# Kernel tuning notes

Measured on AMD Instinct MI355X. Metric: run time of the kernel, lower is better.

## Reference

```python
import jax, jax.numpy as jnp
import numpy as np

N_NODES = 200   # nlim = 50*4
EMB = 5
N_APPTYPES = 3
FEAT_IN = 50 * 52 + N_NODES  # 2800
B = 16384
E = 800


def setup_inputs() -> dict:
    key = jax.random.key(0)
    ks = jax.random.split(key, 16)
    x = jax.random.normal(ks[0], (B, 50, 52), dtype=jnp.float32)
    apps = jax.random.randint(ks[1], (B, N_NODES), 0, N_APPTYPES)
    edge_src = jax.random.randint(ks[2], (E,), 0, N_NODES)
    edge_dst = jax.random.randint(ks[3], (E,), 0, N_NODES)
    def lin(k, fan_in, fan_out):
        bound = 1.0 / np.sqrt(fan_in)
        kw, kb = jax.random.split(k)
        W = jax.random.uniform(kw, (fan_in, fan_out), minval=-bound, maxval=bound, dtype=jnp.float32)
        b = jax.random.uniform(kb, (fan_out,), minval=-bound, maxval=bound, dtype=jnp.float32)
        return W, b
    emb_table = jax.random.normal(ks[4], (N_APPTYPES, EMB), dtype=jnp.float32)
    gc_w, gc_b = lin(ks[5], EMB, 1)
    W1, b1 = lin(ks[6], FEAT_IN, 128)
    W2, b2 = lin(ks[7], 128, 128)
    W3, b3 = lin(ks[8], 128, 64)
    W4, b4 = lin(ks[9], 64, 2)
    return {"x": x, "apps": apps, "edge_src": edge_src, "edge_dst": edge_dst,
            "emb_table": emb_table, "gc_w": gc_w, "gc_b": gc_b,
            "W1": W1, "b1": b1, "W2": W2, "b2": b2,
            "W3": W3, "b3": b3, "W4": W4, "b4": b4}


def _graph_conv(h, edge_src, edge_dst, gc_w, gc_b):
    # DGL GraphConv, norm='both': D_in^{-1/2} A D_out^{-1/2} (X W) + b
    ones = jnp.ones((edge_src.shape[0],), dtype=h.dtype)
    deg_out = jnp.clip(jax.ops.segment_sum(ones, edge_src, num_segments=N_NODES), 1.0)
    deg_in = jnp.clip(jax.ops.segment_sum(ones, edge_dst, num_segments=N_NODES), 1.0)
    norm_src = deg_out ** -0.5  # [N]
    norm_dst = deg_in ** -0.5
    hw = h @ gc_w                       # [B, N, 1] (weight applied first: 5 > 1)
    msg = (hw * norm_src[None, :, None])[:, edge_src, :]      # [B, E, 1]
    agg = jnp.zeros_like(hw).at[:, edge_dst, :].add(msg)      # scatter-add over dst
    return agg * norm_dst[None, :, None] + gc_b


def reference(x, apps, edge_src, edge_dst, emb_table, gc_w, gc_b,
              W1, b1, W2, b2, W3, b3, W4, b4):
    h = emb_table[apps]                 # [B, 200, 5]; apps already length nlim -> zero-pad is no-op
    g = _graph_conv(h, edge_src, edge_dst, gc_w, gc_b)        # [B, 200, 1]
    feat = jnp.concatenate([x.reshape(x.shape[0], -1), g.reshape(g.shape[0], -1)], axis=-1)  # [B, 2800]
    a = jax.nn.softplus(feat @ W1 + b1)
    a = jax.nn.softplus(a @ W2 + b2)
    a = a @ W3 + b3
    a = a - jnp.tanh(a)                 # Tanhshrink
    out = jax.nn.sigmoid(a @ W4 + b4)   # [B, 2]
    return out
```

## Files before the change

kernel.cpp:

```cpp
#include <hip/hip_runtime.h>

#define NNODES 200
#define FEATX  2600
#define FEAT   2800
#define NCH    44
#define N1     128

typedef _Float16 f16;
typedef _Float16 f16x8 __attribute__((ext_vector_type(8)));
typedef float    f32x4 __attribute__((ext_vector_type(4)));

#define W1T_OFF   0u
#define W2T_OFF   720896u
#define W3T_OFF   753664u
#define WG_OFF    770048u
#define B1P_OFF   872448u
#define HW_OFF    872960u
#define WE_OFF    874816u

__device__ __forceinline__ void gl_lds16(const void* g, void* l) {
  __builtin_amdgcn_global_load_lds(
      (const __attribute__((address_space(1))) unsigned int*)g,
      (__attribute__((address_space(3))) unsigned int*)l, 16, 0, 0);
}

__global__ void prep1(const int* __restrict__ esrc, const int* __restrict__ edst,
                      const float* __restrict__ emb, const float* __restrict__ gcw,
                      const float* __restrict__ gcb, const float* __restrict__ W1,
                      const float* __restrict__ b1, char* __restrict__ ws) {
  __shared__ float dg[2][NNODES];
  const int tid = threadIdx.x;
  for (int i = tid; i < 2 * NNODES; i += 256) ((float*)dg)[i] = 0.f;
  __syncthreads();
  for (int e = tid; e < 800; e += 256) {
    atomicAdd(&dg[0][esrc[e]], 1.f);
    atomicAdd(&dg[1][edst[e]], 1.f);
  }
  __syncthreads();
  for (int i = tid; i < 2 * NNODES; i += 256) {
    float* p = (float*)dg + i;
    *p = 1.f / sqrtf(fmaxf(*p, 1.f));
  }
  if (tid < 3) {
    float s = 0.f;
    for (int q = 0; q < 5; ++q) s += emb[tid * 5 + q] * gcw[q];
    ((float*)(ws + HW_OFF))[tid] = s;
  }
  __syncthreads();
  float* we = (float*)(ws + WE_OFF);
  for (int e = tid; e < 800; e += 256)
    we[e] = dg[0][esrc[e]] * dg[1][edst[e]];
  if (tid < 128) {
    float s = 0.f;
    for (int d = 0; d < NNODES; ++d) s += W1[(FEATX + d) * N1 + tid];
    ((float*)(ws + B1P_OFF))[tid] = b1[tid] + gcb[0] * s;
  }
}

__global__ void prepWg(const int* __restrict__ esrc, const int* __restrict__ edst,
                       const float* __restrict__ W1, char* __restrict__ ws) {
  __shared__ int   se[800];
  __shared__ short sd[800];
  __shared__ float swe[800];
  const int n = blockIdx.x;
  const int j = threadIdx.x;
  const float* we = (const float*)(ws + WE_OFF);
  for (int e = j; e < 800; e += 128) {
    se[e] = esrc[e]; sd[e] = (short)edst[e]; swe[e] = we[e];
  }
  __syncthreads();
  float acc = 0.f;
  for (int e = 0; e < 800; ++e) {
    if (se[e] == n) acc += swe[e] * W1[(FEATX + (int)sd[e]) * N1 + j];
  }
  ((float*)(ws + WG_OFF))[n * N1 + j] = acc;
}

__global__ void pack(const float* __restrict__ W1, const float* __restrict__ W2,
                     const float* __restrict__ W3, char* __restrict__ ws) {
  __shared__ __align__(16) char tile[32768];
  const int bid = blockIdx.x, tid = threadIdx.x;
  if (bid < NCH) {
    const float* wg = (const float*)(ws + WG_OFF);
    const int c = tid & 127, kh = tid >> 7;
    for (int kk = kh; kk < 64; kk += 2) {
      const int k = bid * 64 + kk;
      float v;
      if (k < FEATX) v = W1[k * N1 + c];
      else if (k < FEAT) v = wg[(k - FEATX) * N1 + c];
      else v = 0.f;
      *(f16*)(tile + ((c * 128 + kk * 2) ^ ((c & 7) << 4))) = (f16)v;
    }
    __syncthreads();
    char* dst = ws + W1T_OFF + bid * 16384;
    for (int i = 0; i < 4; ++i)
      *(uint4*)(dst + tid * 16 + i * 4096) = *(const uint4*)(tile + tid * 16 + i * 4096);
  } else if (bid == NCH) {
    const int c = tid & 127, kh = tid >> 7;
    for (int k = kh; k < 128; k += 2) {
      const float v = W2[k * 128 + c];
      *(f16*)(tile + ((c * 256 + k * 2) ^ ((c & 7) << 4))) = (f16)v;
    }
    __syncthreads();
    char* dst = ws + W2T_OFF;
    for (int i = 0; i < 8; ++i)
      *(uint4*)(dst + tid * 16 + i * 4096) = *(const uint4*)(tile + tid * 16 + i * 4096);
  } else {
    const int c = tid & 63, kh = tid >> 6;
    for (int k = kh; k < 128; k += 4) {
      const float v = W3[k * 64 + c];
      *(f16*)(tile + ((c * 256 + k * 2) ^ ((c & 7) << 4))) = (f16)v;
    }
    __syncthreads();
    char* dst = ws + W3T_OFF;
    for (int i = 0; i < 4; ++i)
      *(uint4*)(dst + tid * 16 + i * 4096) = *(const uint4*)(tile + tid * 16 + i * 4096);
  }
}

__global__ __launch_bounds__(512, 2)
void fused_main(const float* __restrict__ x, const int* __restrict__ apps,
                const char* __restrict__ ws, const float* __restrict__ b2,
                const float* __restrict__ b3, const float* __restrict__ W4,
                const float* __restrict__ b4, float* __restrict__ out) {
  __shared__ __align__(16) char lds[81920];
  char*  sB    = lds;
  char*  sAct1 = lds + 49152;
  char*  sAct2 = lds + 65536;
  float* sAct3 = (float*)(lds + 49152);

  const int tid  = threadIdx.x;
  const int lane = tid & 63;
  const int w    = tid >> 6;
  const int lrow = lane & 15;
  const int lk   = lane >> 4;
  const int wr   = w >> 1;
  const int wc   = w & 1;
  const int blk  = blockIdx.x;

  const float* hwv = (const float*)(ws + HW_OFF);
  const float hw0 = hwv[0], hw1 = hwv[1], hw2 = hwv[2];

  const int row_g = blk * 64 + wr * 16 + lrow;
  const float* xrow = x + (size_t)row_g * FEATX;
  const int*   irow = apps + (size_t)row_g * NNODES;

  int boff[2][4];
#pragma unroll
  for (int ks = 0; ks < 2; ++ks)
#pragma unroll
    for (int f = 0; f < 4; ++f) {
      const int c = wc * 64 + f * 16 + lrow;
      boff[ks][f] = ((c * 128 + ks * 64 + lk * 16) ^ ((lrow & 7) << 4));
    }

  const f32x4 zed = {0.f, 0.f, 0.f, 0.f};
  f32x4 acc1[4] = {zed, zed, zed, zed};

  auto issueB = [&](int tc, int buf) {
    const char* src = ws + W1T_OFF + (size_t)tc * 16384;
    char* dst = sB + buf * 16384;
#pragma unroll
    for (int r = 0; r < 2; ++r) {
      const int o = r * 8192 + w * 1024;
      gl_lds16(src + o + lane * 16, dst + o);
    }
  };
  auto issueA = [&](int tc, uint4 (&ar)[2][2]) {
#pragma unroll
    for (int ks = 0; ks < 2; ++ks) {
      const int k0 = tc * 64 + ks * 32 + lk * 8;
      const char* p;
      if (k0 + 8 <= FEATX)  p = (const char*)(xrow + k0);
      else if (k0 < FEAT)   p = (const char*)(irow + (k0 - FEATX));
      else                  p = (const char*)xrow;
      ar[ks][0] = *(const uint4*)p;
      ar[ks][1] = *(const uint4*)(p + 16);
    }
  };
  auto cvtA = [&](int t, const uint4 (&ar)[2][2], f16x8 (&af)[2]) {
#pragma unroll
    for (int ks = 0; ks < 2; ++ks) {
      const int k0 = t * 64 + ks * 32 + lk * 8;
      union { uint4 u[2]; unsigned ui[8]; float f[8]; } d;
      d.u[0] = ar[ks][0]; d.u[1] = ar[ks][1];
      union { f16x8 v; f16 h[8]; } r;
      if (k0 + 8 <= FEATX) {
#pragma unroll
        for (int j2 = 0; j2 < 8; ++j2) r.h[j2] = (f16)d.f[j2];
      } else if (k0 < FEAT) {
#pragma unroll
        for (int j2 = 0; j2 < 8; ++j2) {
          const unsigned a = d.ui[j2];
          r.h[j2] = (f16)(a == 0u ? hw0 : (a == 1u ? hw1 : hw2));
        }
      } else {
#pragma unroll
        for (int j2 = 0; j2 < 8; ++j2) r.h[j2] = (f16)0.f;
      }
      af[ks] = r.v;
    }
  };
  auto compute = [&](const f16x8 (&af)[2], int buf) {
    const char* b = sB + buf * 16384;
#pragma unroll
    for (int ks = 0; ks < 2; ++ks)
#pragma unroll
      for (int f = 0; f < 4; ++f) {
        const f16x8 bf = *(const f16x8*)(b + boff[ks][f]);
        acc1[f] = __builtin_amdgcn_mfma_f32_16x16x32_f16(af[ks], bf, acc1[f], 0, 0, 0);
      }
  };

  uint4 arA[2][2], arB[2][2];
  f16x8 af[2];

  issueB(0, 0); issueA(0, arA);
  issueB(1, 1); issueA(1, arB);

  for (int t = 0; t < NCH; t += 2) {
    {
      asm volatile("s_waitcnt vmcnt(6)" ::: "memory");
      __builtin_amdgcn_s_barrier();
      __builtin_amdgcn_sched_barrier(0);
      const int tc = (t + 2 < NCH) ? t + 2 : NCH - 1;
      issueB(tc, (t + 2) % 3);
      cvtA(t, arA, af);
      issueA(tc, arA);
      compute(af, t % 3);
    }
    {
      asm volatile("s_waitcnt vmcnt(6)" ::: "memory");
      __builtin_amdgcn_s_barrier();
      __builtin_amdgcn_sched_barrier(0);
      const int t1 = t + 1;
      const int tc = (t1 + 2 < NCH) ? t1 + 2 : NCH - 1;
      issueB(tc, (t1 + 2) % 3);
      cvtA(t1, arB, af);
      issueA(tc, arB);
      compute(af, t1 % 3);
    }
  }
  __syncthreads();

#pragma unroll
  for (int r = 0; r < 6; ++r) {
    const int o = r * 8192 + w * 1024;
    gl_lds16(ws + W2T_OFF + o + lane * 16, lds + o);
  }

  const float* b1p = (const float*)(ws + B1P_OFF);
#pragma unroll
  for (int f = 0; f < 4; ++f) {
    const int col = wc * 64 + f * 16 + lrow;
    const float bb = b1p[col];
#pragma unroll
    for (int r = 0; r < 4; ++r) {
      const int row = wr * 16 + lk * 4 + r;
      float v = acc1[f][r] + bb;
      v = fmaxf(v, 0.f) + log1pf(expf(-fabsf(v)));
      *(f16*)(sAct1 + ((row * 256 + col * 2) ^ ((row & 7) << 4))) = (f16)v;
    }
  }
  __syncthreads();

  f32x4 acc2[4] = {zed, zed, zed, zed};
#pragma unroll
  for (int ks = 0; ks < 4; ++ks) {
    const int ar = wr * 16 + lrow;
    const f16x8 a2 = *(const f16x8*)(sAct1 + ((ar * 256 + ks * 64 + lk * 16) ^ ((lrow & 7) << 4)));
#pragma unroll
    for (int f = 0; f < 4; ++f) {
      const int c = wc * 64 + f * 16 + lrow;
      const f16x8 bf = *(const f16x8*)(lds + ((c * 256 + ks * 64 + lk * 16) ^ ((lrow & 7) << 4)));
      acc2[f] = __builtin_amdgcn_mfma_f32_16x16x32_f16(a2, bf, acc2[f], 0, 0, 0);
    }
  }
#pragma unroll
  for (int f = 0; f < 4; ++f) {
    const int col = wc * 64 + f * 16 + lrow;
    const float bb = b2[col];
#pragma unroll
    for (int r = 0; r < 4; ++r) {
      const int row = wr * 16 + lk * 4 + r;
      float v = acc2[f][r] + bb;
      v = fmaxf(v, 0.f) + log1pf(expf(-fabsf(v)));
      *(f16*)(sAct2 + ((row * 256 + col * 2) ^ ((row & 7) << 4))) = (f16)v;
    }
  }
  __syncthreads();

  f32x4 acc3[2] = {zed, zed};
  const char* w3p = lds + 32768;
#pragma unroll
  for (int ks = 0; ks < 4; ++ks) {
    const int ar = wr * 16 + lrow;
    const f16x8 a3 = *(const f16x8*)(sAct2 + ((ar * 256 + ks * 64 + lk * 16) ^ ((lrow & 7) << 4)));
#pragma unroll
    for (int f = 0; f < 2; ++f) {
      const int c = wc * 32 + f * 16 + lrow;
      const f16x8 bf = *(const f16x8*)(w3p + ((c * 256 + ks * 64 + lk * 16) ^ ((lrow & 7) << 4)));
      acc3[f] = __builtin_amdgcn_mfma_f32_16x16x32_f16(a3, bf, acc3[f], 0, 0, 0);
    }
  }
#pragma unroll
  for (int f = 0; f < 2; ++f) {
    const int col = wc * 32 + f * 16 + lrow;
    const float bb = b3[col];
#pragma unroll
    for (int r = 0; r < 4; ++r) {
      const int row = wr * 16 + lk * 4 + r;
      const float z = acc3[f][r] + bb;
      sAct3[row * 64 + col] = z - tanhf(z);
    }
  }
  __syncthreads();

  if (tid < 128) {
    const int row = tid >> 1, j = tid & 1;
    float a4 = b4[j];
#pragma unroll 8
    for (int k = 0; k < 64; ++k)
      a4 += sAct3[row * 64 + k] * W4[k * 2 + j];
    out[(size_t)(blk * 64 + row) * 2 + j] = 1.f / (1.f + expf(-a4));
  }
}

extern "C" void kernel_launch(void* const* d_in, const int* in_sizes, int n_in,
                              void* d_out, int out_size, void* d_ws, size_t ws_size,
                              hipStream_t stream) {
  const float* x    = (const float*)d_in[0];
  const int*   apps = (const int*)d_in[1];
  const int*   esrc = (const int*)d_in[2];
  const int*   edst = (const int*)d_in[3];
  const float* emb  = (const float*)d_in[4];
  const float* gcw  = (const float*)d_in[5];
  const float* gcb  = (const float*)d_in[6];
  const float* W1   = (const float*)d_in[7];
  const float* b1   = (const float*)d_in[8];
  const float* W2   = (const float*)d_in[9];
  const float* b2   = (const float*)d_in[10];
  const float* W3   = (const float*)d_in[11];
  const float* b3   = (const float*)d_in[12];
  const float* W4   = (const float*)d_in[13];
  const float* b4   = (const float*)d_in[14];
  char* ws = (char*)d_ws;
  float* out = (float*)d_out;

  hipLaunchKernelGGL(prep1, dim3(1), dim3(256), 0, stream,
                     esrc, edst, emb, gcw, gcb, W1, b1, ws);
  hipLaunchKernelGGL(prepWg, dim3(200), dim3(128), 0, stream, esrc, edst, W1, ws);
  hipLaunchKernelGGL(pack, dim3(46), dim3(256), 0, stream, W1, W2, W3, ws);
  hipLaunchKernelGGL(fused_main, dim3(256), dim3(512), 0, stream,
                     x, apps, ws, b2, b3, W4, b4, out);
}
```

Baseline: 391.4 us.

## Stage W1 in 64KB double-buffered groups and merge graph prep kernels

After: 516.4 us. 1.32x slower.

```diff
diff --git a/kernel.cpp b/kernel.cpp
--- a/kernel.cpp
+++ b/kernel.cpp
@@ -4,6 +4,7 @@
 #define FEATX  2600
 #define FEAT   2800
 #define NCH    44
+#define NGRP   11
 #define N1     128
 
 typedef _Float16 f16;
@@ -16,7 +17,6 @@
 #define WG_OFF    770048u
 #define B1P_OFF   872448u
 #define HW_OFF    872960u
-#define WE_OFF    874816u
 
 __device__ __forceinline__ void gl_lds16(const void* g, void* l) {
   __builtin_amdgcn_global_load_lds(
@@ -24,20 +24,30 @@
       (__attribute__((address_space(3))) unsigned int*)l, 16, 0, 0);
 }
 
-__global__ void prep1(const int* __restrict__ esrc, const int* __restrict__ edst,
-                      const float* __restrict__ emb, const float* __restrict__ gcw,
-                      const float* __restrict__ gcb, const float* __restrict__ W1,
-                      const float* __restrict__ b1, char* __restrict__ ws) {
-  __shared__ float dg[2][NNODES];
+__global__ __launch_bounds__(256)
+void prep(const int* __restrict__ esrc, const int* __restrict__ edst,
+          const float* __restrict__ emb, const float* __restrict__ gcw,
+          const float* __restrict__ gcb, const float* __restrict__ W1,
+          const float* __restrict__ b1, char* __restrict__ ws) {
+  __shared__ float dg[2][256];
+  __shared__ int   se[800];
+  __shared__ int   sd[800];
+  __shared__ float swe[800];
+  __shared__ float wga[NNODES * N1];
+  __shared__ float red[256];
   const int tid = threadIdx.x;
-  for (int i = tid; i < 2 * NNODES; i += 256) ((float*)dg)[i] = 0.f;
+
+  for (int i = tid; i < 512; i += 256) ((float*)dg)[i] = 0.f;
+  for (int i = tid; i < NNODES * N1; i += 256) wga[i] = 0.f;
   __syncthreads();
   for (int e = tid; e < 800; e += 256) {
-    atomicAdd(&dg[0][esrc[e]], 1.f);
-    atomicAdd(&dg[1][edst[e]], 1.f);
-  }
-  __syncthreads();
-  for (int i = tid; i < 2 * NNODES; i += 256) {
+    const int s = esrc[e], d = edst[e];
+    se[e] = s; sd[e] = d;
+    atomicAdd(&dg[0][s], 1.f);
+    atomicAdd(&dg[1][d], 1.f);
+  }
+  __syncthreads();
+  for (int i = tid; i < 512; i += 256) {
     float* p = (float*)dg + i;
     *p = 1.f / sqrtf(fmaxf(*p, 1.f));
   }
@@ -47,33 +57,28 @@
     ((float*)(ws + HW_OFF))[tid] = s;
   }
   __syncthreads();
-  float* we = (float*)(ws + WE_OFF);
   for (int e = tid; e < 800; e += 256)
-    we[e] = dg[0][esrc[e]] * dg[1][edst[e]];
-  if (tid < 128) {
+    swe[e] = dg[0][se[e]] * dg[1][sd[e]];
+  __syncthreads();
+
+  const int j = tid & 127, h = tid >> 7;
+  for (int e = h; e < 800; e += 2) {
+    const float v = swe[e] * W1[(FEATX + sd[e]) * N1 + j];
+    atomicAdd(&wga[se[e] * N1 + j], v);
+  }
+
+  {
     float s = 0.f;
-    for (int d = 0; d < NNODES; ++d) s += W1[(FEATX + d) * N1 + tid];
-    ((float*)(ws + B1P_OFF))[tid] = b1[tid] + gcb[0] * s;
-  }
-}
-
-__global__ void prepWg(const int* __restrict__ esrc, const int* __restrict__ edst,
-                       const float* __restrict__ W1, char* __restrict__ ws) {
-  __shared__ int   se[800];
-  __shared__ short sd[800];
-  __shared__ float swe[800];
-  const int n = blockIdx.x;
-  const int j = threadIdx.x;
-  const float* we = (const float*)(ws + WE_OFF);
-  for (int e = j; e < 800; e += 128) {
-    se[e] = esrc[e]; sd[e] = (short)edst[e]; swe[e] = we[e];
-  }
-  __syncthreads();
-  float acc = 0.f;
-  for (int e = 0; e < 800; ++e) {
-    if (se[e] == n) acc += swe[e] * W1[(FEATX + (int)sd[e]) * N1 + j];
-  }
-  ((float*)(ws + WG_OFF))[n * N1 + j] = acc;
+    for (int d = h; d < NNODES; d += 2)
+      s += W1[(FEATX + d) * N1 + j];
+    red[tid] = s;
+    __syncthreads();
+    if (h == 0)
+      ((float*)(ws + B1P_OFF))[j] = b1[j] + gcb[0] * (red[j] + red[128 + j]);
+  }
+  __syncthreads();
+  float4* dst = (float4*)(ws + WG_OFF);
+  for (int i = tid; i < NNODES * N1 / 4; i += 256) dst[i] = ((const float4*)wga)[i];
 }
 
 __global__ void pack(const float* __restrict__ W1, const float* __restrict__ W2,
@@ -123,8 +128,7 @@
                 const char* __restrict__ ws, const float* __restrict__ b2,
                 const float* __restrict__ b3, const float* __restrict__ W4,
                 const float* __restrict__ b4, float* __restrict__ out) {
-  __shared__ __align__(16) char lds[81920];
-  char*  sB    = lds;
+  __shared__ __align__(16) char lds[131072];
   char*  sAct1 = lds + 49152;
   char*  sAct2 = lds + 65536;
   float* sAct3 = (float*)(lds + 49152);
@@ -157,11 +161,12 @@
   const f32x4 zed = {0.f, 0.f, 0.f, 0.f};
   f32x4 acc1[4] = {zed, zed, zed, zed};
 
-  auto issueB = [&](int tc, int buf) {
-    const char* src = ws + W1T_OFF + (size_t)tc * 16384;
-    char* dst = sB + buf * 16384;
-#pragma unroll
-    for (int r = 0; r < 2; ++r) {
+  auto issueG = [&](int g) {
+    const int gg = (g > NGRP - 1) ? NGRP - 1 : g;
+    const char* src = ws + W1T_OFF + (size_t)(gg * 4) * 16384;
+    char* dst = lds + (g & 1) * 65536;
+#pragma unroll
+    for (int r = 0; r < 8; ++r) {
       const int o = r * 8192 + w * 1024;
       gl_lds16(src + o + lane * 16, dst + o);
     }
@@ -201,8 +206,7 @@
       af[ks] = r.v;
     }
   };
-  auto compute = [&](const f16x8 (&af)[2], int buf) {
-    const char* b = sB + buf * 16384;
+  auto compute = [&](const f16x8 (&af)[2], const char* b) {
 #pragma unroll
     for (int ks = 0; ks < 2; ++ks)
 #pragma unroll
@@ -215,31 +219,32 @@
   uint4 arA[2][2], arB[2][2];
   f16x8 af[2];
 
-  issueB(0, 0); issueA(0, arA);
-  issueB(1, 1); issueA(1, arB);
-
-  for (int t = 0; t < NCH; t += 2) {
-    {
-      asm volatile("s_waitcnt vmcnt(6)" ::: "memory");
-      __builtin_amdgcn_s_barrier();
-      __builtin_amdgcn_sched_barrier(0);
-      const int tc = (t + 2 < NCH) ? t + 2 : NCH - 1;
-      issueB(tc, (t + 2) % 3);
-      cvtA(t, arA, af);
-      issueA(tc, arA);
-      compute(af, t % 3);
-    }
-    {
-      asm volatile("s_waitcnt vmcnt(6)" ::: "memory");
-      __builtin_amdgcn_s_barrier();
-      __builtin_amdgcn_sched_barrier(0);
-      const int t1 = t + 1;
-      const int tc = (t1 + 2 < NCH) ? t1 + 2 : NCH - 1;
-      issueB(tc, (t1 + 2) % 3);
-      cvtA(t1, arB, af);
-      issueA(tc, arB);
-      compute(af, t1 % 3);
-    }
+  issueG(0);
+  __builtin_amdgcn_sched_barrier(0);
+  issueA(0, arA);
+  issueA(1, arB);
+  __builtin_amdgcn_sched_barrier(0);
+
+  for (int g = 0; g < NGRP; ++g) {
+    asm volatile("s_waitcnt vmcnt(8)" ::: "memory");
+    __builtin_amdgcn_s_barrier();
+    __builtin_amdgcn_sched_barrier(0);
+    issueG(g + 1);
+    __builtin_amdgcn_sched_barrier(0);
+    const char* bb = lds + (g & 1) * 65536;
+    const int t0 = 4 * g;
+    cvtA(t0 + 0, arA, af); issueA(t0 + 2, arA);
+    __builtin_amdgcn_sched_barrier(0);
+    compute(af, bb);
+    cvtA(t0 + 1, arB, af); issueA(t0 + 3, arB);
+    __builtin_amdgcn_sched_barrier(0);
+    compute(af, bb + 16384);
+    cvtA(t0 + 2, arA, af); issueA(t0 + 4, arA);
+    __builtin_amdgcn_sched_barrier(0);
+    compute(af, bb + 32768);
+    cvtA(t0 + 3, arB, af); issueA(t0 + 5, arB);
+    __builtin_amdgcn_sched_barrier(0);
+    compute(af, bb + 49152);
   }
   __syncthreads();
 
@@ -303,6 +308,7 @@
       acc3[f] = __builtin_amdgcn_mfma_f32_16x16x32_f16(a3, bf, acc3[f], 0, 0, 0);
     }
   }
+  __syncthreads();
 #pragma unroll
   for (int f = 0; f < 2; ++f) {
     const int col = wc * 32 + f * 16 + lrow;
@@ -316,13 +322,24 @@
   }
   __syncthreads();
 
-  if (tid < 128) {
-    const int row = tid >> 1, j = tid & 1;
-    float a4 = b4[j];
-#pragma unroll 8
-    for (int k = 0; k < 64; ++k)
-      a4 += sAct3[row * 64 + k] * W4[k * 2 + j];
-    out[(size_t)(blk * 64 + row) * 2 + j] = 1.f / (1.f + expf(-a4));
+  if (tid < 256) {
+    const int row = tid >> 2, q = tid & 3;
+    float a0 = 0.f, a1 = 0.f;
+#pragma unroll
+    for (int k = q * 16; k < q * 16 + 16; k += 2) {
+      const float2 a = *(const float2*)(&sAct3[row * 64 + k]);
+      const float4 wv = *(const float4*)(W4 + k * 2);
+      a0 += a.x * wv.x + a.y * wv.z;
+      a1 += a.x * wv.y + a.y * wv.w;
+    }
+    a0 += __shfl_down(a0, 1); a1 += __shfl_down(a1, 1);
+    a0 += __shfl_down(a0, 2); a1 += __shfl_down(a1, 2);
+    if (q == 0) {
+      float2 o;
+      o.x = 1.f / (1.f + expf(-(a0 + b4[0])));
+      o.y = 1.f / (1.f + expf(-(a1 + b4[1])));
+      *(float2*)(out + (size_t)(blk * 64 + row) * 2) = o;
+    }
   }
 }
 
@@ -347,9 +364,8 @@
   char* ws = (char*)d_ws;
   float* out = (float*)d_out;
 
-  hipLaunchKernelGGL(prep1, dim3(1), dim3(256), 0, stream,
+  hipLaunchKernelGGL(prep, dim3(1), dim3(256), 0, stream,
                      esrc, edst, emb, gcw, gcb, W1, b1, ws);
-  hipLaunchKernelGGL(prepWg, dim3(200), dim3(128), 0, stream, esrc, edst, W1, ws);
   hipLaunchKernelGGL(pack, dim3(46), dim3(256), 0, stream, W1, W2, W3, ws);
   hipLaunchKernelGGL(fused_main, dim3(256), dim3(512), 0, stream,
                      x, apps, ws, b2, b3, W4, b4, out);
```
